# Optimization experiments

Hardware: AMD Instinct MI355X
Metric: run time of the kernel (lower is better)

Reference implementation:

```python
import jax, jax.numpy as jnp
import numpy as np

N = 100000
H, C = 2, 16
EPS = 1e-16


def gatv2_conv(x, Wl, Wr, att, bias, src, dst, n):
    # x: [N, Fin]; Wl/Wr: [Fin, H*C]; att: [H, C]; bias: [H*C]
    xl = (x @ Wl).reshape(n, H, C)  # source-side transform
    xr = (x @ Wr).reshape(n, H, C)  # destination-side transform
    # per-edge GATv2 score: a^T LeakyReLU(xl_j + xr_i)
    z = jax.nn.leaky_relu(xl[src] + xr[dst], negative_slope=0.2)  # [E, H, C]
    e = jnp.einsum('ehc,hc->eh', z, att)  # [E, H]
    # softmax over incoming edges per destination node
    m = jax.ops.segment_max(e, dst, num_segments=n)  # [N, H]
    ex = jnp.exp(e - m[dst])
    s = jax.ops.segment_sum(ex, dst, num_segments=n)  # [N, H]
    alpha = ex / (s[dst] + EPS)  # [E, H]
    # scatter-add aggregation of weighted source features
    out = jax.ops.segment_sum(alpha[:, :, None] * xl[src], dst, num_segments=n)  # [N, H, C]
    return out.reshape(n, H * C) + bias


def setup_inputs() -> dict:
    key = jax.random.key(0)
    ks = jax.random.split(key, 12)
    F_in, n_cls, E = 1433, 7, 3200000
    x = jax.random.normal(ks[0], (N, F_in), dtype=jnp.float32)
    edge_index = jax.random.randint(ks[1], (2, E), 0, N, dtype=jnp.int64)
    sc = 0.05
    return {
        'x': x,
        'edge_index': edge_index,
        'Wl1': jax.random.normal(ks[2], (F_in, H * C), dtype=jnp.float32) * sc,
        'Wr1': jax.random.normal(ks[3], (F_in, H * C), dtype=jnp.float32) * sc,
        'a1': jax.random.normal(ks[4], (H, C), dtype=jnp.float32) * sc,
        'b1': jnp.zeros((H * C,), dtype=jnp.float32),
        'Wl2': jax.random.normal(ks[5], (H * C, H * C), dtype=jnp.float32) * sc,
        'Wr2': jax.random.normal(ks[6], (H * C, H * C), dtype=jnp.float32) * sc,
        'a2': jax.random.normal(ks[7], (H, C), dtype=jnp.float32) * sc,
        'b2': jnp.zeros((H * C,), dtype=jnp.float32),
        'fcW': jax.random.normal(ks[8], (H * C, n_cls), dtype=jnp.float32) * sc,
        'fcb': jnp.zeros((n_cls,), dtype=jnp.float32),
    }


def reference(x, edge_index, Wl1, Wr1, a1, b1, Wl2, Wr2, a2, b2, fcW, fcb):
    n = x.shape[0]
    loops = jnp.arange(n, dtype=edge_index.dtype)
    src = jnp.concatenate([edge_index[0], loops])  # add self-loops (PyG default)
    dst = jnp.concatenate([edge_index[1], loops])
    h = jax.nn.elu(gatv2_conv(x, Wl1, Wr1, a1, b1, src, dst, n))
    h = jax.nn.elu(gatv2_conv(h, Wl2, Wr2, a2, b2, src, dst, n))
    logits = h @ fcW + fcb
    return jax.nn.log_softmax(logits, axis=1)
```

## Files before the change

kernel.cpp:

```cpp
#include <hip/hip_runtime.h>
#include <hip/hip_bf16.h>
#include <cstddef>
#include <cstdint>

#define HC 32
#define NHEADS 2
#define CH 16
#define CAP 96

typedef __bf16 bf16x8 __attribute__((ext_vector_type(8)));
typedef float  f32x4  __attribute__((ext_vector_type(4)));

#define BM 128
#define BK 32
#define LDA 40

__global__ __launch_bounds__(256) void gemm_dual_mfma(
    const float* __restrict__ A, int N, int K,
    const float* __restrict__ Wl, const float* __restrict__ Wr,
    float* __restrict__ XL, float* __restrict__ XR)
{
    __shared__ __align__(16) __bf16 Asm[BM * LDA];
    __shared__ __align__(16) __bf16 Wsm[64 * LDA];
    const int tid  = threadIdx.x;
    const int lane = tid & 63;
    const int w    = tid >> 6;
    const int row0 = blockIdx.x * BM;

    f32x4 acc[2][4];
    #pragma unroll
    for (int i = 0; i < 2; ++i)
        #pragma unroll
        for (int j = 0; j < 4; ++j) acc[i][j] = (f32x4){0.f, 0.f, 0.f, 0.f};

    const int frag_m = lane & 15;
    const int frag_k = lane >> 4;

    for (int k0 = 0; k0 < K; k0 += BK) {
        __syncthreads();
        #pragma unroll
        for (int i = 0; i < 8; ++i) {
            int pidx = tid + i * 256;
            int r  = pidx >> 4;
            int kp = (pidx & 15) * 2;
            int gr = row0 + r;
            int gk = k0 + kp;
            float v0 = 0.f, v1 = 0.f;
            if (gr < N) {
                const float* ap = A + (size_t)gr * K + gk;
                if (gk < K)     v0 = ap[0];
                if (gk + 1 < K) v1 = ap[1];
            }
            Asm[r * LDA + kp]     = (__bf16)v0;
            Asm[r * LDA + kp + 1] = (__bf16)v1;
        }
        {
            int kk = tid >> 3;
            int n  = (tid & 7) * 4;
            int gk = k0 + kk;
            float4 vl = make_float4(0.f, 0.f, 0.f, 0.f);
            float4 vr = vl;
            if (gk < K) {
                vl = *(const float4*)(Wl + (size_t)gk * HC + n);
                vr = *(const float4*)(Wr + (size_t)gk * HC + n);
            }
            Wsm[(n + 0) * LDA + kk] = (__bf16)vl.x;
            Wsm[(n + 1) * LDA + kk] = (__bf16)vl.y;
            Wsm[(n + 2) * LDA + kk] = (__bf16)vl.z;
            Wsm[(n + 3) * LDA + kk] = (__bf16)vl.w;
            Wsm[(32 + n + 0) * LDA + kk] = (__bf16)vr.x;
            Wsm[(32 + n + 1) * LDA + kk] = (__bf16)vr.y;
            Wsm[(32 + n + 2) * LDA + kk] = (__bf16)vr.z;
            Wsm[(32 + n + 3) * LDA + kk] = (__bf16)vr.w;
        }
        __syncthreads();
        bf16x8 afrag[2], bfrag[4];
        #pragma unroll
        for (int mt = 0; mt < 2; ++mt)
            afrag[mt] = *(const bf16x8*)&Asm[(w * 32 + mt * 16 + frag_m) * LDA + frag_k * 8];
        #pragma unroll
        for (int nt = 0; nt < 4; ++nt)
            bfrag[nt] = *(const bf16x8*)&Wsm[(nt * 16 + frag_m) * LDA + frag_k * 8];
        #pragma unroll
        for (int mt = 0; mt < 2; ++mt)
            #pragma unroll
            for (int nt = 0; nt < 4; ++nt)
                acc[mt][nt] = __builtin_amdgcn_mfma_f32_16x16x32_bf16(
                    afrag[mt], bfrag[nt], acc[mt][nt], 0, 0, 0);
    }
    const int cl = lane & 15;
    const int rq = (lane >> 4) * 4;
    #pragma unroll
    for (int mt = 0; mt < 2; ++mt) {
        #pragma unroll
        for (int nt = 0; nt < 4; ++nt) {
            int col = nt * 16 + cl;
            float* dst = (col < HC) ? XL : XR;
            int c = (col < HC) ? col : (col - HC);
            #pragma unroll
            for (int r = 0; r < 4; ++r) {
                int grow = row0 + w * 32 + mt * 16 + rq + r;
                if (grow < N) dst[(size_t)grow * HC + c] = acc[mt][nt][r];
            }
        }
    }
}

__global__ __launch_bounds__(256) void gemm_dual(
    const float* __restrict__ A, int N, int K,
    const float* __restrict__ Wl, const float* __restrict__ Wr,
    float* __restrict__ XL, float* __restrict__ XR)
{
    __shared__ __align__(16) float As[64][33];
    __shared__ __align__(16) float Ws[32][68];
    const int tid = threadIdx.x;
    const int tx = tid & 15;
    const int ty = tid >> 4;
    const int row0 = blockIdx.x * 64;

    float acc[4][4];
    #pragma unroll
    for (int i = 0; i < 4; ++i)
        #pragma unroll
        for (int j = 0; j < 4; ++j) acc[i][j] = 0.f;

    for (int k0 = 0; k0 < K; k0 += 32) {
        #pragma unroll
        for (int i = 0; i < 8; ++i) {
            int idx = tid + i * 256;
            int r = idx >> 5;
            int kk = idx & 31;
            int gr = row0 + r, gk = k0 + kk;
            As[r][kk] = (gr < N && gk < K) ? A[(size_t)gr * K + gk] : 0.f;
        }
        #pragma unroll
        for (int i = 0; i < 8; ++i) {
            int idx = tid + i * 256;
            int kk = idx >> 6;
            int c = idx & 63;
            int gk = k0 + kk;
            float v = 0.f;
            if (gk < K) v = (c < HC) ? Wl[(size_t)gk * HC + c]
                                     : Wr[(size_t)gk * HC + (c - HC)];
            Ws[kk][c] = v;
        }
        __syncthreads();
        #pragma unroll
        for (int kk = 0; kk < 32; ++kk) {
            const float4 bv = *(const float4*)(&Ws[kk][tx * 4]);
            float av[4];
            #pragma unroll
            for (int i = 0; i < 4; ++i) av[i] = As[ty * 4 + i][kk];
            #pragma unroll
            for (int i = 0; i < 4; ++i) {
                acc[i][0] = fmaf(av[i], bv.x, acc[i][0]);
                acc[i][1] = fmaf(av[i], bv.y, acc[i][1]);
                acc[i][2] = fmaf(av[i], bv.z, acc[i][2]);
                acc[i][3] = fmaf(av[i], bv.w, acc[i][3]);
            }
        }
        __syncthreads();
    }
    #pragma unroll
    for (int i = 0; i < 4; ++i) {
        int gr = row0 + ty * 4 + i;
        if (gr < N) {
            float4 v = make_float4(acc[i][0], acc[i][1], acc[i][2], acc[i][3]);
            int c0 = tx * 4;
            if (c0 < HC) *(float4*)&XL[(size_t)gr * HC + c0] = v;
            else         *(float4*)&XR[(size_t)gr * HC + (c0 - HC)] = v;
        }
    }
}

__global__ __launch_bounds__(256) void scatter_fixed(
    const int* __restrict__ src, const int* __restrict__ dst,
    int E, int Etot, int* __restrict__ cnt, int* __restrict__ csr_src)
{
    int e = blockIdx.x * blockDim.x + threadIdx.x;
    if (e >= Etot) return;
    int si, di;
    if (e < E) { si = src[e]; di = dst[e]; }
    else       { si = e - E;  di = si; }
    int pos = atomicAdd(&cnt[di], 1);
    if (pos < CAP) csr_src[(size_t)di * CAP + pos] = si;
}

__global__ __launch_bounds__(256) void gather_pass(
    const float* __restrict__ xl, float* __restrict__ xr,
    const float* __restrict__ att, const int* __restrict__ cnt,
    const int* __restrict__ csr_src, const float* __restrict__ bias, int N)
{
    int d = (blockIdx.x * blockDim.x + threadIdx.x) >> 6;
    if (d >= N) return;
    const int lane = threadIdx.x & 63;
    const int c = lane & 31;
    const int eslot = lane >> 5;

    const float xrc  = xr[(size_t)d * HC + c];
    const float attc = att[c];
    const float bc   = bias[c];
    int deg = cnt[d]; if (deg > CAP) deg = CAP;
    const int* __restrict__ row = csr_src + (size_t)d * CAP;

    float accv = 0.f, den = 0.f;
    int p = eslot;
    for (; p + 6 < deg; p += 8) {
        int s0 = row[p], s1 = row[p + 2], s2 = row[p + 4], s3 = row[p + 6];
        float x0 = xl[(size_t)s0 * HC + c];
        float x1 = xl[(size_t)s1 * HC + c];
        float x2 = xl[(size_t)s2 * HC + c];
        float x3 = xl[(size_t)s3 * HC + c];
        float z0 = x0 + xrc; z0 = z0 > 0.f ? z0 : 0.2f * z0;
        float z1 = x1 + xrc; z1 = z1 > 0.f ? z1 : 0.2f * z1;
        float z2 = x2 + xrc; z2 = z2 > 0.f ? z2 : 0.2f * z2;
        float z3 = x3 + xrc; z3 = z3 > 0.f ? z3 : 0.2f * z3;
        float t0 = z0 * attc, t1 = z1 * attc, t2 = z2 * attc, t3 = z3 * attc;
        t0 += __shfl_xor(t0, 1); t1 += __shfl_xor(t1, 1);
        t2 += __shfl_xor(t2, 1); t3 += __shfl_xor(t3, 1);
        t0 += __shfl_xor(t0, 2); t1 += __shfl_xor(t1, 2);
        t2 += __shfl_xor(t2, 2); t3 += __shfl_xor(t3, 2);
        t0 += __shfl_xor(t0, 4); t1 += __shfl_xor(t1, 4);
        t2 += __shfl_xor(t2, 4); t3 += __shfl_xor(t3, 4);
        t0 += __shfl_xor(t0, 8); t1 += __shfl_xor(t1, 8);
        t2 += __shfl_xor(t2, 8); t3 += __shfl_xor(t3, 8);
        float e0 = __expf(t0), e1 = __expf(t1);
        float e2 = __expf(t2), e3 = __expf(t3);
        den += (e0 + e1) + (e2 + e3);
        accv = fmaf(e0, x0, accv);
        accv = fmaf(e1, x1, accv);
        accv = fmaf(e2, x2, accv);
        accv = fmaf(e3, x3, accv);
    }
    for (; p < deg; p += 2) {
        int sid = row[p];
        float x0 = xl[(size_t)sid * HC + c];
        float z = x0 + xrc;
        z = z > 0.f ? z : 0.2f * z;
        float t = z * attc;
        t += __shfl_xor(t, 1);
        t += __shfl_xor(t, 2);
        t += __shfl_xor(t, 4);
        t += __shfl_xor(t, 8);
        float ex = __expf(t);
        den += ex;
        accv = fmaf(ex, x0, accv);
    }
    accv += __shfl_xor(accv, 32);
    den  += __shfl_xor(den, 32);
    if (eslot == 0) {
        float v = accv / (den + 1e-16f) + bc;
        v = v > 0.f ? v : expm1f(v);
        xr[(size_t)d * HC + c] = v;
    }
}

__global__ __launch_bounds__(256) void fc_logsoftmax(
    const float* __restrict__ h, const float* __restrict__ W,
    const float* __restrict__ b, float* __restrict__ out, int N)
{
    int n = blockIdx.x * blockDim.x + threadIdx.x;
    if (n >= N) return;
    float hv[32];
    const float4* h4 = (const float4*)(h + (size_t)n * HC);
    #pragma unroll
    for (int j = 0; j < 8; ++j) {
        float4 t = h4[j];
        hv[j * 4 + 0] = t.x; hv[j * 4 + 1] = t.y;
        hv[j * 4 + 2] = t.z; hv[j * 4 + 3] = t.w;
    }
    float lg[7];
    #pragma unroll
    for (int c = 0; c < 7; ++c) lg[c] = b[c];
    #pragma unroll
    for (int k = 0; k < 32; ++k) {
        float hk = hv[k];
        #pragma unroll
        for (int c = 0; c < 7; ++c) lg[c] = fmaf(hk, W[k * 7 + c], lg[c]);
    }
    float m = lg[0];
    #pragma unroll
    for (int c = 1; c < 7; ++c) m = fmaxf(m, lg[c]);
    float sum = 0.f;
    #pragma unroll
    for (int c = 0; c < 7; ++c) sum += expf(lg[c] - m);
    float lse = m + logf(sum);
    #pragma unroll
    for (int c = 0; c < 7; ++c) out[(size_t)n * 7 + c] = lg[c] - lse;
}

extern "C" void kernel_launch(void* const* d_in, const int* in_sizes, int n_in,
                              void* d_out, int out_size, void* d_ws, size_t ws_size,
                              hipStream_t stream) {
    const float* x   = (const float*)d_in[0];
    const int*   ei  = (const int*)d_in[1];
    const float* Wl1 = (const float*)d_in[2];
    const float* Wr1 = (const float*)d_in[3];
    const float* a1  = (const float*)d_in[4];
    const float* b1  = (const float*)d_in[5];
    const float* Wl2 = (const float*)d_in[6];
    const float* Wr2 = (const float*)d_in[7];
    const float* a2  = (const float*)d_in[8];
    const float* b2  = (const float*)d_in[9];
    const float* fcW = (const float*)d_in[10];
    const float* fcb = (const float*)d_in[11];
    float* out = (float*)d_out;

    const int Fin  = 1433;
    const int N    = in_sizes[0] / Fin;
    const int E    = in_sizes[1] / 2;
    const int Etot = E + N;

    float* xl      = (float*)d_ws;
    float* xr      = xl + (size_t)N * HC;
    int*   cnt     = (int*)(xr + (size_t)N * HC);
    int*   csr_src = cnt + N;

    const int* srcp = ei;
    const int* dstp = ei + E;

    dim3 blk(256);
    dim3 gM((N + BM - 1) / BM);
    dim3 gN64((N + 63) / 64);
    dim3 gE((Etot + 255) / 256);
    dim3 gW((N * 64 + 255) / 256);
    dim3 gN((N + 255) / 256);

    hipMemsetAsync(cnt, 0, (size_t)N * sizeof(int), stream);
    scatter_fixed<<<gE, blk, 0, stream>>>(srcp, dstp, E, Etot, cnt, csr_src);

    gemm_dual_mfma<<<gM, blk, 0, stream>>>(x, N, Fin, Wl1, Wr1, xl, xr);
    gather_pass<<<gW, blk, 0, stream>>>(xl, xr, a1, cnt, csr_src, b1, N);
    gemm_dual<<<gN64, blk, 0, stream>>>(xr, N, HC, Wl2, Wr2, xl, xr);
    gather_pass<<<gW, blk, 0, stream>>>(xl, xr, a2, cnt, csr_src, b2, N);
    fc_logsoftmax<<<gN, blk, 0, stream>>>(xr, fcW, fcb, out, N);
}
```

Before: 1.433 ms.

## Load GEMM fragments directly from global memory using pre-transposed bf16 weights

A small prep kernel transposes and converts Wl1/Wr1 into a padded bf16 [64, 1440] layout. The large first-layer GEMM then drops its shared-memory staging and the two __syncthreads per K step. Each lane loads its A row fragment straight from global memory as unaligned float4 vectors and its B fragments from the prepared weights, with a separate tail step for the leftover K. This removes the LDS round-trip and barriers on a bandwidth-bound GEMM. In exchange it relies on unaligned vector loads and lane-strided access to A rows, which may coalesce worse, and it adds an extra kernel launch.

```diff
diff --git a/kernel.cpp b/kernel.cpp
--- a/kernel.cpp
+++ b/kernel.cpp
@@ -8,86 +8,105 @@
 #define CH 16
 #define CAP 96
 
+#define KK    1433
+#define KFULL 1408
+#define WTP   1440
+
 typedef __bf16 bf16x8 __attribute__((ext_vector_type(8)));
 typedef float  f32x4  __attribute__((ext_vector_type(4)));
+typedef float  f32x4u __attribute__((ext_vector_type(4), aligned(4)));
 
 #define BM 128
-#define BK 32
-#define LDA 40
+
+__global__ __launch_bounds__(256) void wprep(
+    const float* __restrict__ Wl, const float* __restrict__ Wr,
+    __bf16* __restrict__ Wt)
+{
+    int idx = blockIdx.x * 256 + threadIdx.x;
+    if (idx >= 64 * WTP) return;
+    int n = idx / WTP;
+    int k = idx - n * WTP;
+    float v = 0.f;
+    if (k < KK) v = (n < HC) ? Wl[(size_t)k * HC + n]
+                             : Wr[(size_t)k * HC + (n - HC)];
+    Wt[idx] = (__bf16)v;
+}
 
 __global__ __launch_bounds__(256) void gemm_dual_mfma(
-    const float* __restrict__ A, int N, int K,
-    const float* __restrict__ Wl, const float* __restrict__ Wr,
+    const float* __restrict__ A, int N,
+    const __bf16* __restrict__ Wt,
     float* __restrict__ XL, float* __restrict__ XR)
 {
-    __shared__ __align__(16) __bf16 Asm[BM * LDA];
-    __shared__ __align__(16) __bf16 Wsm[64 * LDA];
     const int tid  = threadIdx.x;
     const int lane = tid & 63;
     const int w    = tid >> 6;
     const int row0 = blockIdx.x * BM;
-
-    f32x4 acc[2][4];
-    #pragma unroll
-    for (int i = 0; i < 2; ++i)
-        #pragma unroll
-        for (int j = 0; j < 4; ++j) acc[i][j] = (f32x4){0.f, 0.f, 0.f, 0.f};
-
     const int frag_m = lane & 15;
     const int frag_k = lane >> 4;
 
-    for (int k0 = 0; k0 < K; k0 += BK) {
-        __syncthreads();
-        #pragma unroll
-        for (int i = 0; i < 8; ++i) {
-            int pidx = tid + i * 256;
-            int r  = pidx >> 4;
-            int kp = (pidx & 15) * 2;
-            int gr = row0 + r;
-            int gk = k0 + kp;
-            float v0 = 0.f, v1 = 0.f;
-            if (gr < N) {
-                const float* ap = A + (size_t)gr * K + gk;
-                if (gk < K)     v0 = ap[0];
-                if (gk + 1 < K) v1 = ap[1];
-            }
-            Asm[r * LDA + kp]     = (__bf16)v0;
-            Asm[r * LDA + kp + 1] = (__bf16)v1;
-        }
-        {
-            int kk = tid >> 3;
-            int n  = (tid & 7) * 4;
-            int gk = k0 + kk;
-            float4 vl = make_float4(0.f, 0.f, 0.f, 0.f);
-            float4 vr = vl;
-            if (gk < K) {
-                vl = *(const float4*)(Wl + (size_t)gk * HC + n);
-                vr = *(const float4*)(Wr + (size_t)gk * HC + n);
-            }
-            Wsm[(n + 0) * LDA + kk] = (__bf16)vl.x;
-            Wsm[(n + 1) * LDA + kk] = (__bf16)vl.y;
-            Wsm[(n + 2) * LDA + kk] = (__bf16)vl.z;
-            Wsm[(n + 3) * LDA + kk] = (__bf16)vl.w;
-            Wsm[(32 + n + 0) * LDA + kk] = (__bf16)vr.x;
-            Wsm[(32 + n + 1) * LDA + kk] = (__bf16)vr.y;
-            Wsm[(32 + n + 2) * LDA + kk] = (__bf16)vr.z;
-            Wsm[(32 + n + 3) * LDA + kk] = (__bf16)vr.w;
-        }
-        __syncthreads();
-        bf16x8 afrag[2], bfrag[4];
-        #pragma unroll
-        for (int mt = 0; mt < 2; ++mt)
-            afrag[mt] = *(const bf16x8*)&Asm[(w * 32 + mt * 16 + frag_m) * LDA + frag_k * 8];
+    f32x4 acc[2][4];
+    #pragma unroll
+    for (int i = 0; i < 2; ++i)
+        #pragma unroll
+        for (int j = 0; j < 4; ++j) acc[i][j] = (f32x4){0.f, 0.f, 0.f, 0.f};
+
+    int r0 = row0 + w * 32 + frag_m;
+    int r1 = r0 + 16;
+    int cr0 = (r0 < N) ? r0 : N - 1;
+    int cr1 = (r1 < N) ? r1 : N - 1;
+    const float* __restrict__ a0 = A + (size_t)cr0 * KK + frag_k * 8;
+    const float* __restrict__ a1 = A + (size_t)cr1 * KK + frag_k * 8;
+    const __bf16* __restrict__ wb = Wt + (size_t)frag_m * WTP + frag_k * 8;
+
+    #pragma unroll 4
+    for (int k0 = 0; k0 < KFULL; k0 += 32) {
+        f32x4u u0 = *(const f32x4u*)(a0 + k0);
+        f32x4u u1 = *(const f32x4u*)(a0 + k0 + 4);
+        f32x4u v0 = *(const f32x4u*)(a1 + k0);
+        f32x4u v1 = *(const f32x4u*)(a1 + k0 + 4);
+        bf16x8 bfv[4];
         #pragma unroll
         for (int nt = 0; nt < 4; ++nt)
-            bfrag[nt] = *(const bf16x8*)&Wsm[(nt * 16 + frag_m) * LDA + frag_k * 8];
-        #pragma unroll
-        for (int mt = 0; mt < 2; ++mt)
-            #pragma unroll
-            for (int nt = 0; nt < 4; ++nt)
-                acc[mt][nt] = __builtin_amdgcn_mfma_f32_16x16x32_bf16(
-                    afrag[mt], bfrag[nt], acc[mt][nt], 0, 0, 0);
-    }
+            bfv[nt] = *(const bf16x8*)(wb + (size_t)(nt * 16) * WTP + k0);
+        bf16x8 af0, af1;
+        #pragma unroll
+        for (int j = 0; j < 4; ++j) {
+            af0[j]     = (__bf16)u0[j];
+            af0[j + 4] = (__bf16)u1[j];
+            af1[j]     = (__bf16)v0[j];
+            af1[j + 4] = (__bf16)v1[j];
+        }
+        #pragma unroll
+        for (int nt = 0; nt < 4; ++nt) {
+            acc[0][nt] = __builtin_amdgcn_mfma_f32_16x16x32_bf16(
+                af0, bfv[nt], acc[0][nt], 0, 0, 0);
+            acc[1][nt] = __builtin_amdgcn_mfma_f32_16x16x32_bf16(
+                af1, bfv[nt], acc[1][nt], 0, 0, 0);
+        }
+    }
+
+    {
+        bf16x8 af0, af1, bfv[4];
+        #pragma unroll
+        for (int j = 0; j < 8; ++j) {
+            int k = KFULL + frag_k * 8 + j;
+            float x0 = (k < KK) ? a0[KFULL + j] : 0.f;
+            float x1 = (k < KK) ? a1[KFULL + j] : 0.f;
+            af0[j] = (__bf16)x0;
+            af1[j] = (__bf16)x1;
+        }
+        #pragma unroll
+        for (int nt = 0; nt < 4; ++nt)
+            bfv[nt] = *(const bf16x8*)(wb + (size_t)(nt * 16) * WTP + KFULL);
+        #pragma unroll
+        for (int nt = 0; nt < 4; ++nt) {
+            acc[0][nt] = __builtin_amdgcn_mfma_f32_16x16x32_bf16(
+                af0, bfv[nt], acc[0][nt], 0, 0, 0);
+            acc[1][nt] = __builtin_amdgcn_mfma_f32_16x16x32_bf16(
+                af1, bfv[nt], acc[1][nt], 0, 0, 0);
+        }
+    }
+
     const int cl = lane & 15;
     const int rq = (lane >> 4) * 4;
     #pragma unroll
@@ -311,10 +330,11 @@
     const int E    = in_sizes[1] / 2;
     const int Etot = E + N;
 
-    float* xl      = (float*)d_ws;
-    float* xr      = xl + (size_t)N * HC;
-    int*   cnt     = (int*)(xr + (size_t)N * HC);
-    int*   csr_src = cnt + N;
+    float*  xl      = (float*)d_ws;
+    float*  xr      = xl + (size_t)N * HC;
+    int*    cnt     = (int*)(xr + (size_t)N * HC);
+    int*    csr_src = cnt + N;
+    __bf16* Wt      = (__bf16*)(csr_src + (size_t)N * CAP);
 
     const int* srcp = ei;
     const int* dstp = ei + E;
@@ -325,11 +345,13 @@
     dim3 gE((Etot + 255) / 256);
     dim3 gW((N * 64 + 255) / 256);
     dim3 gN((N + 255) / 256);
-
+    dim3 gWp((64 * WTP + 255) / 256);
+
+    wprep<<<gWp, blk, 0, stream>>>(Wl1, Wr1, Wt);
     hipMemsetAsync(cnt, 0, (size_t)N * sizeof(int), stream);
     scatter_fixed<<<gE, blk, 0, stream>>>(srcp, dstp, E, Etot, cnt, csr_src);
 
-    gemm_dual_mfma<<<gM, blk, 0, stream>>>(x, N, Fin, Wl1, Wr1, xl, xr);
+    gemm_dual_mfma<<<gM, blk, 0, stream>>>(x, N, Wt, xl, xr);
     gather_pass<<<gW, blk, 0, stream>>>(xl, xr, a1, cnt, csr_src, b1, N);
     gemm_dual<<<gN64, blk, 0, stream>>>(xr, N, HC, Wl2, Wr2, xl, xr);
     gather_pass<<<gW, blk, 0, stream>>>(xl, xr, a2, cnt, csr_src, b2, N);
```

New measurement: 1.343 ms. 1.07x faster.
